# Optimization experiments

Measured on AMD Instinct MI355X. Metric: run time of the kernel, lower is better.

The kernel has to match this reference:

```python
import jax, jax.numpy as jnp
import numpy as np
import math

B, N_AGENT, E = 32, 64, 256        # batch, agents, n_embd
DV, NV, HIS, DK = 32, 8, 50, 9     # head dim, heads, his_length, action_dim+1


def positional_encoding(max_seq_len, d_model):
    position = jnp.arange(max_seq_len, dtype=jnp.float32)[:, None]
    div_term = jnp.exp(jnp.arange(0, d_model, 2, dtype=jnp.float32) * (-math.log(10000.0) / d_model))
    pe = jnp.zeros((max_seq_len, d_model), jnp.float32)
    pe = pe.at[:, 0::2].set(jnp.sin(position * div_term))
    pe = pe.at[:, 1::2].set(jnp.cos(position * div_term))
    return pe


def setup_inputs() -> dict:
    key = jax.random.key(0)
    ks = jax.random.split(key, 12)
    q = jax.random.normal(ks[0], (B, N_AGENT, E), jnp.float32)
    k = jax.random.normal(ks[1], (B, HIS, N_AGENT, DK), jnp.float32)
    # adjacency: one-hot row selecting, per (agent, timestep), which agent's action to gather
    idx = jax.random.randint(ks[2], (N_AGENT, HIS), 0, N_AGENT)
    adjs_pos = jax.nn.one_hot(idx, N_AGENT, dtype=jnp.float32)  # [N, HIS, N]
    s = 0.05
    return {
        "q": q,
        "k": k,
        "adjs_pos": adjs_pos,
        "Wq": s * jax.random.normal(ks[3], (E, DV * NV), jnp.float32),
        "bq": jnp.zeros((DV * NV,), jnp.float32),
        "Wk": s * jax.random.normal(ks[4], (E, DV * NV), jnp.float32),
        "bk": jnp.zeros((DV * NV,), jnp.float32),
        "Wv": s * jax.random.normal(ks[5], (E, DV * NV), jnp.float32),
        "bv": jnp.zeros((DV * NV,), jnp.float32),
        "Wout": s * jax.random.normal(ks[6], (DV * NV, E), jnp.float32),
        "bout": jnp.zeros((E,), jnp.float32),
        "Wenc": s * jax.random.normal(ks[7], (DK, E), jnp.float32),
    }


def reference(q, k, adjs_pos, Wq, bq, Wk, bk, Wv, bv, Wout, bout, Wenc):
    b, n, e = q.shape
    d_k = k.shape[-1]  # torch code scales by sqrt(k.size(-1)) = 9
    pe = positional_encoding(HIS, e)  # [HIS, E]

    # query head: relu(Linear) then split heads -> [B, N, NV, DV]
    qh = jax.nn.relu(q @ Wq + bq).reshape(b, n, NV, DV)

    # adjacency gather: one-hot matmul selecting a neighbor's action per (agent, t)
    # avoids materializing the repeated [B,N,HIS,N,DK] tensor
    neigh = jnp.einsum('ntA,btAd->bntd', adjs_pos, k)  # [B, N, HIS, DK]

    # action encoder (GELU, exact erf as in nn.GELU) + positional encoding
    neigh = jax.nn.gelu(neigh @ Wenc, approximate=False) + pe  # [B, N, HIS, E]

    # key/value heads
    kh = jax.nn.relu(neigh @ Wk + bk).reshape(b, n, HIS, NV, DV)
    vh = jax.nn.relu(neigh @ Wv + bv).reshape(b, n, HIS, NV, DV)

    # attention over the history axis
    att = jnp.einsum('bnvd,bntvd->bnvt', qh, kh) / jnp.sqrt(jnp.float32(d_k))
    att = jax.nn.softmax(att, axis=-1)  # [B, N, NV, HIS]

    out = jnp.einsum('bnvt,bntvd->bnvd', att, vh).reshape(b, n, NV * DV)
    return jax.nn.relu(out @ Wout + bout)  # [B, N, E]
```

## Files before the change

kernel.cpp:

```cpp
#include <hip/hip_runtime.h>
#include <math.h>

#define NB   32
#define NA   64
#define EDIM 256
#define HIS  50
#define DKA  9
#define NV   8

typedef _Float16 HALF;
typedef _Float16 half4 __attribute__((ext_vector_type(4)));
typedef _Float16 half8 __attribute__((ext_vector_type(8)));
typedef float    f32x4 __attribute__((ext_vector_type(4)));

#define WS_WKP   0
#define WS_WVP   131072
#define WS_WQP   262144
#define WS_WOP   393216
#define WS_PE    524288
#define WS_IDX   575488
#define WS_QH    588288
#define WS_NEED  1636864ULL

__device__ __forceinline__ float gelu_exact(float x) {
    const float ax = fabsf(x) * 0.70710678118654752f;
    const float t  = __builtin_amdgcn_rcpf(1.0f + 0.3275911f * ax);
    const float p  = t * (0.254829592f + t * (-0.284496736f + t * (1.421413741f
                   + t * (-1.453152027f + t * 1.061405429f))));
    const float er = 1.0f - p * __expf(-ax * ax);
    return 0.5f * x * (1.0f + copysignf(er, x));
}

__global__ __launch_bounds__(256) void pack_setup(
    const float* __restrict__ Wk, const float* __restrict__ Wv,
    const float* __restrict__ Wq, const float* __restrict__ Wout,
    const float* __restrict__ adjs,
    char* __restrict__ ws)
{
    const int tid = blockIdx.x * 256 + threadIdx.x;
    HALF* WkP  = (HALF*)(ws + WS_WKP);
    HALF* WvP  = (HALF*)(ws + WS_WVP);
    HALF* WqP  = (HALF*)(ws + WS_WQP);
    HALF* WoP  = (HALF*)(ws + WS_WOP);
    float* PE  = (float*)(ws + WS_PE);
    int*  idxT = (int*)(ws + WS_IDX);

    {
        const int elem = tid & 7;
        const int lane = (tid >> 3) & 63;
        const int kt   = (tid >> 9) & 7;
        const int nt   = tid >> 12;
        const int k = kt * 32 + (lane >> 4) * 8 + elem;
        const int n = nt * 16 + (lane & 15);
        WkP[tid] = (HALF)Wk[k * EDIM + n];
        WvP[tid] = (HALF)Wv[k * EDIM + n];
        WqP[tid] = (HALF)Wq[k * EDIM + n];
        WoP[tid] = (HALF)Wout[k * EDIM + n];
    }
    if (tid < HIS * EDIM) {
        const int t = tid >> 8;
        const int e = tid & 255;
        const float dt = expf(-(float)(e & ~1) * (9.210340371976184f / 256.0f));
        const float arg = (float)t * dt;
        PE[tid] = (e & 1) ? cosf(arg) : sinf(arg);
    }
    if (tid < NA * HIS) {
        const float* row = adjs + tid * NA;
        int best = 0;
        #pragma unroll
        for (int a = 0; a < NA; ++a) best = (row[a] > 0.5f) ? a : best;
        idxT[tid] = best;
    }
}

__global__ __launch_bounds__(256) void qh_gemm(
    const float* __restrict__ q,
    const float* __restrict__ bq,
    const char*  __restrict__ ws,
    char* __restrict__ wsout)
{
    const int tid = threadIdx.x, lane = tid & 63, w = tid >> 6;
    const int l15 = lane & 15, l4 = lane >> 4;
    const int bx  = blockIdx.x;
    const int r0  = (bx >> 1) * 64;
    const int nh  = bx & 1;
    const HALF* WqP = (const HALF*)(ws + WS_WQP);
    HALF* qh = (HALF*)(wsout + WS_QH);

    f32x4 acc[4][2];
    #pragma unroll
    for (int mt = 0; mt < 4; ++mt)
        #pragma unroll
        for (int nt = 0; nt < 2; ++nt) acc[mt][nt] = (f32x4)0.0f;

    #pragma unroll 2
    for (int kk = 0; kk < 8; ++kk) {
        half8 afr[4];
        #pragma unroll
        for (int mt = 0; mt < 4; ++mt) {
            const float* ap = &q[(size_t)(r0 + mt * 16 + l15) * EDIM + kk * 32 + l4 * 8];
            const float4 a0 = *reinterpret_cast<const float4*>(ap);
            const float4 a1 = *reinterpret_cast<const float4*>(ap + 4);
            half8 h;
            h[0] = (HALF)a0.x; h[1] = (HALF)a0.y; h[2] = (HALF)a0.z; h[3] = (HALF)a0.w;
            h[4] = (HALF)a1.x; h[5] = (HALF)a1.y; h[6] = (HALF)a1.z; h[7] = (HALF)a1.w;
            afr[mt] = h;
        }
        #pragma unroll
        for (int nt = 0; nt < 2; ++nt) {
            const int ntile = nh * 8 + w * 2 + nt;
            const half8 bfr = *reinterpret_cast<const half8*>(
                WqP + ((size_t)(ntile * 8 + kk) * 64 + lane) * 8);
            #pragma unroll
            for (int mt = 0; mt < 4; ++mt)
                acc[mt][nt] = __builtin_amdgcn_mfma_f32_16x16x32_f16(afr[mt], bfr, acc[mt][nt], 0, 0, 0);
        }
    }

    #pragma unroll
    for (int nt = 0; nt < 2; ++nt) {
        const int col = (nh * 8 + w * 2 + nt) * 16 + l15;
        const float bqa = bq[col];
        #pragma unroll
        for (int mt = 0; mt < 4; ++mt)
            #pragma unroll
            for (int r = 0; r < 4; ++r) {
                const int row = l4 * 4 + r;
                qh[(size_t)(r0 + mt * 16 + row) * EDIM + col] =
                    (HALF)fmaxf(acc[mt][nt][r] + bqa, 0.0f);
            }
    }
}

__global__ __launch_bounds__(512, 4) void attn_fused(
    const float* __restrict__ kin,
    const float* __restrict__ bk,
    const float* __restrict__ bv,
    const float* __restrict__ Wenc,
    const char*  __restrict__ ws,
    char* __restrict__ wsout)
{
    const int tid  = threadIdx.x;
    const int lane = tid & 63;
    const int w    = tid >> 6;
    const int l15  = lane & 15;
    const int l4   = lane >> 4;
    const int bidx = blockIdx.x;
    const int b = bidx >> 6, n = bidx & 63;

    const HALF* WkP  = (const HALF*)(ws + WS_WKP);
    const HALF* WvP  = (const HALF*)(ws + WS_WVP);
    const HALF* qh   = (const HALF*)(ws + WS_QH);
    const float* PE  = (const float*)(ws + WS_PE);
    const int*  idxT = (const int*)(ws + WS_IDX);
    HALF* O = (HALF*)(wsout + WS_QH);

    __shared__ __align__(16) HALF  s_A[32 * 64 * 8];
    __shared__ __align__(16) float s_neigh[HIS][12];
    __shared__ float s_att[NV][64];
    __shared__ __align__(16) float s_o[EDIM];

    for (int i = tid; i < HIS * 12; i += 512) {
        const int t = i / 12;
        const int d = i - t * 12;
        float val = 0.0f;
        if (d < DKA) val = kin[((b * HIS + t) * NA + idxT[n * HIS + t]) * DKA + d];
        s_neigh[t][d] = val;
    }
    __syncthreads();

    {
        const int c4   = tid & 63;
        const int slot = tid >> 6;
        const int e0   = c4 * 4;
        const int kk   = e0 >> 5;
        const int fg   = (e0 >> 3) & 3;
        const int sub  = (e0 >> 2) & 1;
        float4 we[DKA];
        #pragma unroll
        for (int d = 0; d < DKA; ++d)
            we[d] = *reinterpret_cast<const float4*>(&Wenc[d * EDIM + e0]);

        for (int t = slot; t < HIS; t += 8) {
            float4 x = s_neigh[t][0] * we[0];
            #pragma unroll
            for (int d = 1; d < DKA; ++d) x += s_neigh[t][d] * we[d];
            const float4 pe = *reinterpret_cast<const float4*>(&PE[t * EDIM + e0]);
            half4 hv;
            hv[0] = (HALF)(gelu_exact(x.x) + pe.x);
            hv[1] = (HALF)(gelu_exact(x.y) + pe.y);
            hv[2] = (HALF)(gelu_exact(x.z) + pe.z);
            hv[3] = (HALF)(gelu_exact(x.w) + pe.w);
            const int row = kk * 4 + (t >> 4);
            const int fl  = fg * 16 + (t & 15);
            *reinterpret_cast<half4*>(&s_A[(row * 64 + (fl ^ kk)) * 8 + sub * 4]) = hv;
        }
        const half8 z = (half8)(HALF)0.0f;
        for (int i = tid; i < 8 * 4 * 14; i += 512) {
            const int kz  = i / 56;
            const int rem = i - kz * 56;
            const int fgz = rem / 14;
            const int tz  = 2 + (rem - fgz * 14);
            const int flz = fgz * 16 + tz;
            *reinterpret_cast<half8*>(&s_A[((kz * 4 + 3) * 64 + (flz ^ kz)) * 8]) = z;
        }
    }
    __syncthreads();

    float qv[2], bkb[2], bvb[2];
    #pragma unroll
    for (int nt = 0; nt < 2; ++nt) {
        const int col = w * 32 + nt * 16 + l15;
        qv[nt]  = (float)qh[(size_t)bidx * EDIM + col];
        bkb[nt] = bk[col];
        bvb[nt] = bv[col];
    }

    f32x4 ka[4][2], va[4][2];
    #pragma unroll
    for (int mt = 0; mt < 4; ++mt)
        #pragma unroll
        for (int nt = 0; nt < 2; ++nt) { ka[mt][nt] = (f32x4)0.0f; va[mt][nt] = (f32x4)0.0f; }

    #pragma unroll
    for (int kk = 0; kk < 8; ++kk) {
        half8 afr[4];
        #pragma unroll
        for (int mt = 0; mt < 4; ++mt)
            afr[mt] = *reinterpret_cast<const half8*>(
                &s_A[((kk * 4 + mt) * 64 + (lane ^ kk)) * 8]);
        #pragma unroll
        for (int nt = 0; nt < 2; ++nt) {
            const size_t boff = ((size_t)((w * 2 + nt) * 8 + kk) * 64 + lane) * 8;
            const half8 bkfr = *reinterpret_cast<const half8*>(WkP + boff);
            const half8 bvfr = *reinterpret_cast<const half8*>(WvP + boff);
            #pragma unroll
            for (int mt = 0; mt < 4; ++mt) {
                ka[mt][nt] = __builtin_amdgcn_mfma_f32_16x16x32_f16(afr[mt], bkfr, ka[mt][nt], 0, 0, 0);
                va[mt][nt] = __builtin_amdgcn_mfma_f32_16x16x32_f16(afr[mt], bvfr, va[mt][nt], 0, 0, 0);
            }
        }
    }

    #pragma unroll
    for (int mt = 0; mt < 4; ++mt)
        #pragma unroll
        for (int r = 0; r < 4; ++r) {
            float p = qv[0] * fmaxf(ka[mt][0][r] + bkb[0], 0.0f)
                    + qv[1] * fmaxf(ka[mt][1][r] + bkb[1], 0.0f);
            p += __shfl_xor(p, 1);
            p += __shfl_xor(p, 2);
            p += __shfl_xor(p, 4);
            p += __shfl_xor(p, 8);
            if (l15 == 0) s_att[w][mt * 16 + l4 * 4 + r] = p * (1.0f / 3.0f);
        }

    {
        const float val = (lane < HIS) ? s_att[w][lane] : -1e30f;
        float m = val;
        m = fmaxf(m, __shfl_xor(m, 1));
        m = fmaxf(m, __shfl_xor(m, 2));
        m = fmaxf(m, __shfl_xor(m, 4));
        m = fmaxf(m, __shfl_xor(m, 8));
        m = fmaxf(m, __shfl_xor(m, 16));
        m = fmaxf(m, __shfl_xor(m, 32));
        const float e = (lane < HIS) ? __expf(val - m) : 0.0f;
        float s = e;
        s += __shfl_xor(s, 1);
        s += __shfl_xor(s, 2);
        s += __shfl_xor(s, 4);
        s += __shfl_xor(s, 8);
        s += __shfl_xor(s, 16);
        s += __shfl_xor(s, 32);
        s_att[w][lane] = e * __builtin_amdgcn_rcpf(s) * (s * __builtin_amdgcn_rcpf(s));
        s_att[w][lane] = e / s;
    }

    {
        float o0 = 0.f, o1 = 0.f;
        #pragma unroll
        for (int mt = 0; mt < 4; ++mt)
            #pragma unroll
            for (int r = 0; r < 4; ++r) {
                const int t = mt * 16 + l4 * 4 + r;
                const float a = s_att[w][t];
                o0 += a * fmaxf(va[mt][0][r] + bvb[0], 0.0f);
                o1 += a * fmaxf(va[mt][1][r] + bvb[1], 0.0f);
            }
        o0 += __shfl_xor(o0, 16); o1 += __shfl_xor(o1, 16);
        o0 += __shfl_xor(o0, 32); o1 += __shfl_xor(o1, 32);
        if (lane < 16) {
            s_o[w * 32 +  0 + l15] = o0;
            s_o[w * 32 + 16 + l15] = o1;
        }
    }
    __syncthreads();

    if (tid < 256) O[(size_t)bidx * EDIM + tid] = (HALF)s_o[tid];
}

__global__ __launch_bounds__(256) void out_gemm(
    const float* __restrict__ bout,
    const char*  __restrict__ ws,
    float* __restrict__ out)
{
    const int tid = threadIdx.x, lane = tid & 63, w = tid >> 6;
    const int l15 = lane & 15, l4 = lane >> 4;
    const int bx  = blockIdx.x;
    const int r0  = (bx >> 1) * 64;
    const int nh  = bx & 1;
    const HALF* WoP = (const HALF*)(ws + WS_WOP);
    const HALF* O   = (const HALF*)(ws + WS_QH);

    f32x4 acc[4][2];
    #pragma unroll
    for (int mt = 0; mt < 4; ++mt)
        #pragma unroll
        for (int nt = 0; nt < 2; ++nt) acc[mt][nt] = (f32x4)0.0f;

    #pragma unroll 2
    for (int kk = 0; kk < 8; ++kk) {
        half8 afr[4];
        #pragma unroll
        for (int mt = 0; mt < 4; ++mt)
            afr[mt] = *reinterpret_cast<const half8*>(
                &O[(size_t)(r0 + mt * 16 + l15) * EDIM + kk * 32 + l4 * 8]);
        #pragma unroll
        for (int nt = 0; nt < 2; ++nt) {
            const int ntile = nh * 8 + w * 2 + nt;
            const half8 bfr = *reinterpret_cast<const half8*>(
                WoP + ((size_t)(ntile * 8 + kk) * 64 + lane) * 8);
            #pragma unroll
            for (int mt = 0; mt < 4; ++mt)
                acc[mt][nt] = __builtin_amdgcn_mfma_f32_16x16x32_f16(afr[mt], bfr, acc[mt][nt], 0, 0, 0);
        }
    }

    #pragma unroll
    for (int nt = 0; nt < 2; ++nt) {
        const int col = (nh * 8 + w * 2 + nt) * 16 + l15;
        const float boa = bout[col];
        #pragma unroll
        for (int mt = 0; mt < 4; ++mt)
            #pragma unroll
            for (int r = 0; r < 4; ++r) {
                const int row = l4 * 4 + r;
                out[(size_t)(r0 + mt * 16 + row) * EDIM + col] =
                    fmaxf(acc[mt][nt][r] + boa, 0.0f);
            }
    }
}

__global__ __launch_bounds__(256) void mha_fallback(
    const float* __restrict__ q,
    const float* __restrict__ kin,
    const float* __restrict__ adjs,
    const float* __restrict__ Wq, const float* __restrict__ bq,
    const float* __restrict__ Wk, const float* __restrict__ bk,
    const float* __restrict__ Wv, const float* __restrict__ bv,
    const float* __restrict__ Wout, const float* __restrict__ bout,
    const float* __restrict__ Wenc,
    float* __restrict__ out)
{
    const int tid  = threadIdx.x;
    const int bidx = blockIdx.x;
    const int b = bidx >> 6;
    const int n = bidx & 63;

    __shared__ __align__(16) float s_q[EDIM];
    __shared__ __align__(16) float s_qh[EDIM];
    __shared__ __align__(16) float s_neigh[HIS][12];
    __shared__ __align__(16) float s_enc[HIS * EDIM];
    __shared__ float s_att[NV][66];
    __shared__ __align__(16) float s_opart[4][EDIM];
    __shared__ __align__(16) float s_o[EDIM];
    __shared__ int s_idx[HIS];

    s_q[tid] = q[bidx * EDIM + tid];
    if (tid < HIS) {
        const float* row = adjs + (n * HIS + tid) * NA;
        int best = 0;
        #pragma unroll
        for (int a = 0; a < NA; ++a) best = (row[a] > 0.5f) ? a : best;
        s_idx[tid] = best;
    }
    __syncthreads();

    for (int i = tid; i < HIS * 12; i += 256) {
        const int t = i / 12;
        const int d = i - t * 12;
        float val = 0.0f;
        if (d < DKA) val = kin[((b * HIS + t) * NA + s_idx[t]) * DKA + d];
        s_neigh[t][d] = val;
    }
    __syncthreads();

    {
        const int e = tid;
        float acc = bq[e];
        #pragma unroll 4
        for (int d0 = 0; d0 < EDIM; d0 += 4) {
            const float4 qv = *reinterpret_cast<const float4*>(&s_q[d0]);
            acc += qv.x * Wq[(d0 + 0) * EDIM + e];
            acc += qv.y * Wq[(d0 + 1) * EDIM + e];
            acc += qv.z * Wq[(d0 + 2) * EDIM + e];
            acc += qv.w * Wq[(d0 + 3) * EDIM + e];
        }
        s_qh[e] = fmaxf(acc, 0.0f);

        float we[12];
        #pragma unroll
        for (int j = 0; j < 12; ++j) we[j] = (j < DKA) ? Wenc[j * EDIM + e] : 0.0f;
        const float dt = expf(-(float)(e & ~1) * (9.210340371976184f / 256.0f));
        for (int t = 0; t < HIS; ++t) {
            const float4 n0 = *reinterpret_cast<const float4*>(&s_neigh[t][0]);
            const float4 n1 = *reinterpret_cast<const float4*>(&s_neigh[t][4]);
            const float4 n2 = *reinterpret_cast<const float4*>(&s_neigh[t][8]);
            float x = n0.x*we[0] + n0.y*we[1] + n0.z*we[2] + n0.w*we[3]
                    + n1.x*we[4] + n1.y*we[5] + n1.z*we[6] + n1.w*we[7]
                    + n2.x*we[8];
            x = 0.5f * x * (1.0f + erff(x * 0.70710678118654752f));
            const float arg = (float)t * dt;
            const float pe = (e & 1) ? cosf(arg) : sinf(arg);
            s_enc[t * EDIM + e] = x + pe;
        }
    }
    __syncthreads();

    const int g = tid & 63;
    const int h = tid >> 6;
    const int tbase  = (h == 0) ? 0 : (h == 1) ? 13 : (h == 2) ? 25 : 37;
    const int tcount = (h == 1 || h == 2) ? 12 : 13;
    const int v = g >> 3;

    {
        float4 kacc[13];
        const float4 bkv = *reinterpret_cast<const float4*>(&bk[4 * g]);
        #pragma unroll
        for (int tt = 0; tt < 13; ++tt) kacc[tt] = bkv;
        #pragma unroll 2
        for (int d0 = 0; d0 < EDIM; d0 += 4) {
            const float4 w0 = *reinterpret_cast<const float4*>(&Wk[(d0 + 0) * EDIM + 4 * g]);
            const float4 w1 = *reinterpret_cast<const float4*>(&Wk[(d0 + 1) * EDIM + 4 * g]);
            const float4 w2 = *reinterpret_cast<const float4*>(&Wk[(d0 + 2) * EDIM + 4 * g]);
            const float4 w3 = *reinterpret_cast<const float4*>(&Wk[(d0 + 3) * EDIM + 4 * g]);
            #pragma unroll
            for (int tt = 0; tt < 13; ++tt) {
                const float4 ev = *reinterpret_cast<const float4*>(&s_enc[(tbase + tt) * EDIM + d0]);
                kacc[tt].x += ev.x * w0.x + ev.y * w1.x + ev.z * w2.x + ev.w * w3.x;
                kacc[tt].y += ev.x * w0.y + ev.y * w1.y + ev.z * w2.y + ev.w * w3.y;
                kacc[tt].z += ev.x * w0.z + ev.y * w1.z + ev.z * w2.z + ev.w * w3.z;
                kacc[tt].w += ev.x * w0.w + ev.y * w1.w + ev.z * w2.w + ev.w * w3.w;
            }
        }
        const float4 qv = *reinterpret_cast<const float4*>(&s_qh[4 * g]);
        #pragma unroll
        for (int tt = 0; tt < 13; ++tt) {
            float p = qv.x * fmaxf(kacc[tt].x, 0.0f)
                    + qv.y * fmaxf(kacc[tt].y, 0.0f)
                    + qv.z * fmaxf(kacc[tt].z, 0.0f)
                    + qv.w * fmaxf(kacc[tt].w, 0.0f);
            p += __shfl_xor(p, 1);
            p += __shfl_xor(p, 2);
            p += __shfl_xor(p, 4);
            if ((g & 7) == 0) s_att[v][tbase + tt] = p * (1.0f / 3.0f);
        }
    }
    __syncthreads();

    if (tid < NV) {
        float m = -1e30f;
        for (int t = 0; t < HIS; ++t) m = fmaxf(m, s_att[tid][t]);
        float ssum = 0.0f;
        for (int t = 0; t < HIS; ++t) {
            const float ex = expf(s_att[tid][t] - m);
            s_att[tid][t] = ex;
            ssum += ex;
        }
        const float inv = 1.0f / ssum;
        for (int t = 0; t < HIS; ++t) s_att[tid][t] *= inv;
    }
    __syncthreads();

    {
        float4 vacc[13];
        const float4 bvv = *reinterpret_cast<const float4*>(&bv[4 * g]);
        #pragma unroll
        for (int tt = 0; tt < 13; ++tt) vacc[tt] = bvv;
        #pragma unroll 2
        for (int d0 = 0; d0 < EDIM; d0 += 4) {
            const float4 w0 = *reinterpret_cast<const float4*>(&Wv[(d0 + 0) * EDIM + 4 * g]);
            const float4 w1 = *reinterpret_cast<const float4*>(&Wv[(d0 + 1) * EDIM + 4 * g]);
            const float4 w2 = *reinterpret_cast<const float4*>(&Wv[(d0 + 2) * EDIM + 4 * g]);
            const float4 w3 = *reinterpret_cast<const float4*>(&Wv[(d0 + 3) * EDIM + 4 * g]);
            #pragma unroll
            for (int tt = 0; tt < 13; ++tt) {
                const float4 ev = *reinterpret_cast<const float4*>(&s_enc[(tbase + tt) * EDIM + d0]);
                vacc[tt].x += ev.x * w0.x + ev.y * w1.x + ev.z * w2.x + ev.w * w3.x;
                vacc[tt].y += ev.x * w0.y + ev.y * w1.y + ev.z * w2.y + ev.w * w3.y;
                vacc[tt].z += ev.x * w0.z + ev.y * w1.z + ev.z * w2.z + ev.w * w3.z;
                vacc[tt].w += ev.x * w0.w + ev.y * w1.w + ev.z * w2.w + ev.w * w3.w;
            }
        }
        float4 po = make_float4(0.0f, 0.0f, 0.0f, 0.0f);
        #pragma unroll
        for (int tt = 0; tt < 13; ++tt) {
            if (tt < tcount) {
                const float a = s_att[v][tbase + tt];
                po.x += a * fmaxf(vacc[tt].x, 0.0f);
                po.y += a * fmaxf(vacc[tt].y, 0.0f);
                po.z += a * fmaxf(vacc[tt].z, 0.0f);
                po.w += a * fmaxf(vacc[tt].w, 0.0f);
            }
        }
        *reinterpret_cast<float4*>(&s_opart[h][4 * g]) = po;
    }
    __syncthreads();

    s_o[tid] = s_opart[0][tid] + s_opart[1][tid] + s_opart[2][tid] + s_opart[3][tid];
    __syncthreads();

    {
        const int e = tid;
        float acc = bout[e];
        #pragma unroll 4
        for (int d0 = 0; d0 < EDIM; d0 += 4) {
            const float4 ov = *reinterpret_cast<const float4*>(&s_o[d0]);
            acc += ov.x * Wout[(d0 + 0) * EDIM + e];
            acc += ov.y * Wout[(d0 + 1) * EDIM + e];
            acc += ov.z * Wout[(d0 + 2) * EDIM + e];
            acc += ov.w * Wout[(d0 + 3) * EDIM + e];
        }
        out[bidx * EDIM + e] = fmaxf(acc, 0.0f);
    }
}

extern "C" void kernel_launch(void* const* d_in, const int* in_sizes, int n_in,
                              void* d_out, int out_size, void* d_ws, size_t ws_size,
                              hipStream_t stream) {
    const float* q    = (const float*)d_in[0];
    const float* kin  = (const float*)d_in[1];
    const float* adjs = (const float*)d_in[2];
    const float* Wq   = (const float*)d_in[3];
    const float* bq   = (const float*)d_in[4];
    const float* Wk   = (const float*)d_in[5];
    const float* bk   = (const float*)d_in[6];
    const float* Wv   = (const float*)d_in[7];
    const float* bv   = (const float*)d_in[8];
    const float* Wout = (const float*)d_in[9];
    const float* bout = (const float*)d_in[10];
    const float* Wenc = (const float*)d_in[11];
    float* out = (float*)d_out;
    char* ws = (char*)d_ws;

    if (ws_size >= WS_NEED) {
        hipLaunchKernelGGL(pack_setup, dim3(256), dim3(256), 0, stream,
                           Wk, Wv, Wq, Wout, adjs, ws);
        hipLaunchKernelGGL(qh_gemm, dim3(64), dim3(256), 0, stream,
                           q, bq, ws, ws);
        hipLaunchKernelGGL(attn_fused, dim3(NB * NA), dim3(512), 0, stream,
                           kin, bk, bv, Wenc, ws, ws);
        hipLaunchKernelGGL(out_gemm, dim3(64), dim3(256), 0, stream,
                           bout, ws, out);
    } else {
        hipLaunchKernelGGL(mha_fallback, dim3(NB * NA), dim3(256), 0, stream,
                           q, kin, adjs, Wq, bq, Wk, bk, Wv, bv, Wout, bout, Wenc, out);
    }
}
```

Measured before the change: 83.26 us.

## Compute action-encoder projection with MFMA and store PE/Wenc as fp16

Replaces the scalar float4 FMA loop that projects gathered neighbor actions through Wenc with a 16x16x32 fp16 MFMA, using a Wenc matrix pre-packed and zero-padded in the setup kernel. The positional encoding table is also stored as fp16 to halve its load traffic. Shared memory is cut by aliasing the neighbor buffer with the output buffer, which needs an extra barrier, and the zero-padding loop is replaced by writing zeros for out-of-range timesteps. The softmax normalisation drops the redundant double computation. Rounding PE and Wenc to fp16 adds some precision loss.

```diff
diff --git a/kernel.cpp b/kernel.cpp
--- a/kernel.cpp
+++ b/kernel.cpp
@@ -17,10 +17,11 @@
 #define WS_WVP   131072
 #define WS_WQP   262144
 #define WS_WOP   393216
-#define WS_PE    524288
-#define WS_IDX   575488
-#define WS_QH    588288
-#define WS_NEED  1636864ULL
+#define WS_PEH   524288
+#define WS_WET   549888
+#define WS_IDX   566272
+#define WS_QH    579072
+#define WS_NEED  1627648ULL
 
 __device__ __forceinline__ float gelu_exact(float x) {
     const float ax = fabsf(x) * 0.70710678118654752f;
@@ -34,7 +35,7 @@
 __global__ __launch_bounds__(256) void pack_setup(
     const float* __restrict__ Wk, const float* __restrict__ Wv,
     const float* __restrict__ Wq, const float* __restrict__ Wout,
-    const float* __restrict__ adjs,
+    const float* __restrict__ adjs, const float* __restrict__ Wenc,
     char* __restrict__ ws)
 {
     const int tid = blockIdx.x * 256 + threadIdx.x;
@@ -42,7 +43,8 @@
     HALF* WvP  = (HALF*)(ws + WS_WVP);
     HALF* WqP  = (HALF*)(ws + WS_WQP);
     HALF* WoP  = (HALF*)(ws + WS_WOP);
-    float* PE  = (float*)(ws + WS_PE);
+    HALF* PEH  = (HALF*)(ws + WS_PEH);
+    HALF* WET  = (HALF*)(ws + WS_WET);
     int*  idxT = (int*)(ws + WS_IDX);
 
     {
@@ -62,7 +64,15 @@
         const int e = tid & 255;
         const float dt = expf(-(float)(e & ~1) * (9.210340371976184f / 256.0f));
         const float arg = (float)t * dt;
-        PE[tid] = (e & 1) ? cosf(arg) : sinf(arg);
+        PEH[tid] = (HALF)((e & 1) ? cosf(arg) : sinf(arg));
+    }
+    if (tid < 16 * 64 * 8) {
+        const int j    = tid & 7;
+        const int lane = (tid >> 3) & 63;
+        const int me   = tid >> 9;
+        const int k = (lane >> 4) * 8 + j;
+        const int e = me * 16 + (lane & 15);
+        WET[tid] = (k < DKA) ? (HALF)Wenc[k * EDIM + e] : (HALF)0.0f;
     }
     if (tid < NA * HIS) {
         const float* row = adjs + tid * NA;
@@ -136,7 +146,6 @@
     const float* __restrict__ kin,
     const float* __restrict__ bk,
     const float* __restrict__ bv,
-    const float* __restrict__ Wenc,
     const char*  __restrict__ ws,
     char* __restrict__ wsout)
 {
@@ -150,62 +159,18 @@
 
     const HALF* WkP  = (const HALF*)(ws + WS_WKP);
     const HALF* WvP  = (const HALF*)(ws + WS_WVP);
+    const HALF* PEH  = (const HALF*)(ws + WS_PEH);
+    const HALF* WET  = (const HALF*)(ws + WS_WET);
     const HALF* qh   = (const HALF*)(ws + WS_QH);
-    const float* PE  = (const float*)(ws + WS_PE);
     const int*  idxT = (const int*)(ws + WS_IDX);
     HALF* O = (HALF*)(wsout + WS_QH);
 
-    __shared__ __align__(16) HALF  s_A[32 * 64 * 8];
-    __shared__ __align__(16) float s_neigh[HIS][12];
+    __shared__ __align__(16) HALF  s_A[16384];
+    __shared__ __align__(16) float s_un[1280];
     __shared__ float s_att[NV][64];
-    __shared__ __align__(16) float s_o[EDIM];
-
-    for (int i = tid; i < HIS * 12; i += 512) {
-        const int t = i / 12;
-        const int d = i - t * 12;
-        float val = 0.0f;
-        if (d < DKA) val = kin[((b * HIS + t) * NA + idxT[n * HIS + t]) * DKA + d];
-        s_neigh[t][d] = val;
-    }
-    __syncthreads();
-
-    {
-        const int c4   = tid & 63;
-        const int slot = tid >> 6;
-        const int e0   = c4 * 4;
-        const int kk   = e0 >> 5;
-        const int fg   = (e0 >> 3) & 3;
-        const int sub  = (e0 >> 2) & 1;
-        float4 we[DKA];
-        #pragma unroll
-        for (int d = 0; d < DKA; ++d)
-            we[d] = *reinterpret_cast<const float4*>(&Wenc[d * EDIM + e0]);
-
-        for (int t = slot; t < HIS; t += 8) {
-            float4 x = s_neigh[t][0] * we[0];
-            #pragma unroll
-            for (int d = 1; d < DKA; ++d) x += s_neigh[t][d] * we[d];
-            const float4 pe = *reinterpret_cast<const float4*>(&PE[t * EDIM + e0]);
-            half4 hv;
-            hv[0] = (HALF)(gelu_exact(x.x) + pe.x);
-            hv[1] = (HALF)(gelu_exact(x.y) + pe.y);
-            hv[2] = (HALF)(gelu_exact(x.z) + pe.z);
-            hv[3] = (HALF)(gelu_exact(x.w) + pe.w);
-            const int row = kk * 4 + (t >> 4);
-            const int fl  = fg * 16 + (t & 15);
-            *reinterpret_cast<half4*>(&s_A[(row * 64 + (fl ^ kk)) * 8 + sub * 4]) = hv;
-        }
-        const half8 z = (half8)(HALF)0.0f;
-        for (int i = tid; i < 8 * 4 * 14; i += 512) {
-            const int kz  = i / 56;
-            const int rem = i - kz * 56;
-            const int fgz = rem / 14;
-            const int tz  = 2 + (rem - fgz * 14);
-            const int flz = fgz * 16 + tz;
-            *reinterpret_cast<half8*>(&s_A[((kz * 4 + 3) * 64 + (flz ^ kz)) * 8]) = z;
-        }
-    }
-    __syncthreads();
+
+    HALF*  s_ng = (HALF*)s_un;
+    float* s_o  = s_un;
 
     float qv[2], bkb[2], bvb[2];
     #pragma unroll
@@ -215,6 +180,65 @@
         bkb[nt] = bk[col];
         bvb[nt] = bv[col];
     }
+
+    #pragma unroll
+    for (int i0 = 0; i0 < 64 * 32; i0 += 512) {
+        const int i = i0 + tid;
+        const int t = i >> 5;
+        const int d = i & 31;
+        float v = 0.0f;
+        if (t < HIS && d < DKA)
+            v = kin[((b * HIS + t) * NA + idxT[n * HIS + t]) * DKA + d];
+        s_ng[t * 40 + d] = (HALF)v;
+    }
+    __syncthreads();
+
+    {
+        half8 aW[2];
+        #pragma unroll
+        for (int mi = 0; mi < 2; ++mi)
+            aW[mi] = *reinterpret_cast<const half8*>(WET + ((size_t)(2 * w + mi) * 64 + lane) * 8);
+
+        f32x4 accE[2][4];
+        #pragma unroll
+        for (int mi = 0; mi < 2; ++mi)
+            #pragma unroll
+            for (int nt = 0; nt < 4; ++nt) accE[mi][nt] = (f32x4)0.0f;
+
+        #pragma unroll
+        for (int nt = 0; nt < 4; ++nt) {
+            const half8 bN = *reinterpret_cast<const half8*>(&s_ng[(nt * 16 + l15) * 40 + l4 * 8]);
+            #pragma unroll
+            for (int mi = 0; mi < 2; ++mi)
+                accE[mi][nt] = __builtin_amdgcn_mfma_f32_16x16x32_f16(aW[mi], bN, accE[mi][nt], 0, 0, 0);
+        }
+
+        const int t_l = l4 & 1;
+        #pragma unroll
+        for (int mi = 0; mi < 2; ++mi) {
+            const int me = 2 * w + mi;
+            const int e0 = me * 16 + l4 * 4;
+            const int fg = mi * 2 + (l4 >> 1);
+            #pragma unroll
+            for (int nt = 0; nt < 4; ++nt) {
+                const int t = nt * 16 + l15;
+                half4 hv;
+                if (t < HIS) {
+                    const half4 pe = *reinterpret_cast<const half4*>(PEH + t * EDIM + e0);
+                    hv[0] = (HALF)(gelu_exact(accE[mi][nt][0]) + (float)pe[0]);
+                    hv[1] = (HALF)(gelu_exact(accE[mi][nt][1]) + (float)pe[1]);
+                    hv[2] = (HALF)(gelu_exact(accE[mi][nt][2]) + (float)pe[2]);
+                    hv[3] = (HALF)(gelu_exact(accE[mi][nt][3]) + (float)pe[3]);
+                } else {
+                    hv[0] = (HALF)0.0f; hv[1] = (HALF)0.0f;
+                    hv[2] = (HALF)0.0f; hv[3] = (HALF)0.0f;
+                }
+                const int gran = (w * 4 + nt) * 64 + ((fg * 16 + l15) ^ w);
+                *reinterpret_cast<half4*>(&s_A[gran * 8 + t_l * 4]) = hv;
+            }
+        }
+    }
+    __syncthreads();
 
     f32x4 ka[4][2], va[4][2];
     #pragma unroll
@@ -272,8 +296,7 @@
         s += __shfl_xor(s, 8);
         s += __shfl_xor(s, 16);
         s += __shfl_xor(s, 32);
-        s_att[w][lane] = e * __builtin_amdgcn_rcpf(s) * (s * __builtin_amdgcn_rcpf(s));
-        s_att[w][lane] = e / s;
+        s_att[w][lane] = e * __builtin_amdgcn_rcpf(s);
     }
 
     {
@@ -289,6 +312,7 @@
             }
         o0 += __shfl_xor(o0, 16); o1 += __shfl_xor(o1, 16);
         o0 += __shfl_xor(o0, 32); o1 += __shfl_xor(o1, 32);
+        __syncthreads();
         if (lane < 16) {
             s_o[w * 32 +  0 + l15] = o0;
             s_o[w * 32 + 16 + l15] = o1;
@@ -555,11 +579,11 @@
 
     if (ws_size >= WS_NEED) {
         hipLaunchKernelGGL(pack_setup, dim3(256), dim3(256), 0, stream,
-                           Wk, Wv, Wq, Wout, adjs, ws);
+                           Wk, Wv, Wq, Wout, adjs, Wenc, ws);
         hipLaunchKernelGGL(qh_gemm, dim3(64), dim3(256), 0, stream,
                            q, bq, ws, ws);
         hipLaunchKernelGGL(attn_fused, dim3(NB * NA), dim3(512), 0, stream,
-                           kin, bk, bv, Wenc, ws, ws);
+                           kin, bk, bv, ws, ws);
         hipLaunchKernelGGL(out_gemm, dim3(64), dim3(256), 0, stream,
                            bout, ws, out);
     } else {
```

Result: no change. 82.60 us (-0.8%).
